# Kernel tuning notes

Measured on AMD Instinct MI355X. Metric: run time of the kernel, lower is better.

The kernel has to match this reference:

```python
import jax, jax.numpy as jnp
import numpy as np

B, ENC, T, DIM, VOCAB = 16, 512, 64, 768, 21128
SCALE = 1.0 / np.sqrt(DIM)
NEG = -1e30
EPS = 1e-6


def setup_inputs() -> dict:
    key = jax.random.key(0)
    ks = jax.random.split(key, 20)
    def lin(k, out_f, in_f):
        k1, k2 = jax.random.split(k)
        bound = 1.0 / np.sqrt(in_f)
        W = jax.random.uniform(k1, (out_f, in_f), jnp.float32, -bound, bound)
        b = jax.random.uniform(k2, (out_f,), jnp.float32, -bound, bound)
        return W, b
    W_r, b_r = lin(ks[5], DIM, 3 * DIM)
    W_u, b_u = lin(ks[6], DIM, 3 * DIM)
    W_c, b_c = lin(ks[7], DIM, 3 * DIM)
    W_out, b_out = lin(ks[8], DIM, DIM)
    W_copy, b_copy = lin(ks[9], DIM, DIM)
    W_mode, b_mode = lin(ks[10], 1, DIM)
    return {
        "input_ids": jax.random.randint(ks[0], (B, ENC), 0, VOCAB, dtype=jnp.int32),
        "input_context": jax.random.normal(ks[1], (B, ENC, DIM), jnp.float32),
        "context_mask": jnp.ones((B, ENC), jnp.float32),
        "decode_input": jax.random.randint(ks[2], (B, T), 0, VOCAB, dtype=jnp.int32),
        "decode_target": jax.random.randint(ks[3], (B, T), 0, VOCAB, dtype=jnp.int32),
        "use_beam_search": 0,
        "beam_width": 1,
        "emb_W": jax.random.normal(ks[4], (VOCAB, DIM), jnp.float32) * 0.02,
        "W_r": W_r, "b_r": b_r,
        "W_u": W_u, "b_u": b_u,
        "W_c": W_c, "b_c": b_c,
        "W_out": W_out, "b_out": b_out,
        "W_copy": W_copy, "b_copy": b_copy,
        "W_mode": W_mode, "b_mode": b_mode,
        "init_h": jax.random.normal(ks[11], (1, DIM), jnp.float32) * 0.02,
    }


def _decode(input_ids, input_context, context_mask, decode_emb, emb_W,
            W_r, b_r, W_u, b_u, W_c, b_c, W_out, b_out, W_copy, b_copy,
            W_mode, b_mode, init_h):
    mask_add = (1.0 - context_mask) * NEG  # (B, ENC)
    rows = jnp.arange(B)[:, None]

    def step(h, emb_t):
        # attention over encoder context
        score = jnp.einsum('bsd,bd->bs', input_context, h) * SCALE + mask_add
        attn = jax.nn.softmax(score, axis=-1)
        attn_vec = jnp.einsum('bs,bsd->bd', attn, input_context)
        x = jnp.concatenate([attn_vec, emb_t, h], axis=-1)  # (B, 3*DIM)
        r = jax.nn.sigmoid(x @ W_r.T + b_r)
        u = jax.nn.sigmoid(x @ W_u.T + b_u)
        xc = jnp.concatenate([attn_vec, emb_t, r * h], axis=-1)
        c = jnp.tanh(xc @ W_c.T + b_c)
        h_new = (1.0 - u) * h + u * c
        # generate distribution (tied embedding softmax)
        out = h_new @ W_out.T + b_out
        vocab_prob = jax.nn.softmax(out @ emb_W.T, axis=-1)  # (B, VOCAB)
        # copy distribution over source positions
        copy_q = h_new @ W_copy.T + b_copy
        copy_logits = jnp.einsum('bd,bsd->bs', copy_q, input_context) + mask_add
        input_prob = jax.nn.softmax(copy_logits, axis=-1)
        mode = jax.nn.sigmoid(h_new @ W_mode.T + b_mode)  # (B, 1)
        vp = vocab_prob * mode
        vp = vp.at[rows, input_ids].add(input_prob * (1.0 - mode))
        return h_new, vp

    h0 = jnp.broadcast_to(init_h, (B, DIM))
    _, probs = jax.lax.scan(step, h0, decode_emb)  # probs: (T, B, VOCAB)
    return probs


def reference(input_ids, input_context, context_mask, decode_input, decode_target,
              use_beam_search, beam_width, emb_W, W_r, b_r, W_u, b_u, W_c, b_c,
              W_out, b_out, W_copy, b_copy, W_mode, b_mode, init_h):
    decode_emb = jnp.transpose(emb_W[decode_input], (1, 0, 2))  # (T, B, DIM)
    probs = _decode(input_ids, input_context, context_mask, decode_emb, emb_W,
                    W_r, b_r, W_u, b_u, W_c, b_c, W_out, b_out, W_copy, b_copy,
                    W_mode, b_mode, init_h)
    predict = jnp.transpose(probs, (1, 0, 2)).reshape(-1, VOCAB)  # (B*T, VOCAB)
    tgt = decode_target.reshape(-1)
    p = predict[jnp.arange(tgt.shape[0]), tgt]
    nz = (tgt != 0).astype(jnp.float32)
    loss = jnp.sum(-jnp.log(p + EPS) * nz) / jnp.sum(nz)
    return jnp.full((B,), loss)
```

## Files before the change

### kernel.cpp

```cpp
#include <hip/hip_runtime.h>
#include <hip/hip_bf16.h>
#include <math.h>

#define Bdim 16
#define ENC 512
#define Tn 64
#define DIM 768
#define VOCAB 21128
#define SCALEF 0.03608439182435161f
#define NEGF   -1e30f
#define NBLK 256
#define DYN_LDS (100 * 1024)

__device__ __forceinline__ float wred_sum(float v) {
#pragma unroll
  for (int m = 32; m >= 1; m >>= 1) v += __shfl_xor(v, m, 64);
  return v;
}
__device__ __forceinline__ float sigmf(float x) { return 1.0f / (1.0f + __expf(-x)); }

__device__ __forceinline__ void astore(float* p, float v) {
  __hip_atomic_store(p, v, __ATOMIC_RELAXED, __HIP_MEMORY_SCOPE_AGENT);
}
__device__ __forceinline__ void astore2(float* p, float a, float b) {
  float2 v = make_float2(a, b);
  __hip_atomic_store((unsigned long long*)p, *(unsigned long long*)&v,
                     __ATOMIC_RELAXED, __HIP_MEMORY_SCOPE_AGENT);
}
__device__ __forceinline__ float aloadf(const float* p) {
  return __hip_atomic_load(const_cast<float*>(p), __ATOMIC_RELAXED, __HIP_MEMORY_SCOPE_AGENT);
}
__device__ __forceinline__ unsigned afadd(unsigned* p) {
  return __hip_atomic_fetch_add(p, 1u, __ATOMIC_RELAXED, __HIP_MEMORY_SCOPE_AGENT);
}
__device__ __forceinline__ unsigned aloadu(const unsigned* p) {
  return __hip_atomic_load(const_cast<unsigned*>(p), __ATOMIC_RELAXED, __HIP_MEMORY_SCOPE_AGENT);
}

__device__ __forceinline__ void gbar(unsigned* leaf, unsigned* root, int idx, int xcd) {
  __syncthreads();
  if (threadIdx.x == 0) {
    asm volatile("s_waitcnt vmcnt(0)" ::: "memory");
    unsigned prev = afadd(&leaf[(idx * 8 + xcd) * 16]);
    if (((prev + 1u) & 31u) == 0u) afadd(&root[idx * 16]);
    while (aloadu(&root[idx * 16]) < 8u) __builtin_amdgcn_s_sleep(1);
  }
  __syncthreads();
}
__device__ __forceinline__ void lbar(unsigned* lbc, int xcd, unsigned tgt) {
  __syncthreads();
  if (threadIdx.x == 0) {
    asm volatile("s_waitcnt vmcnt(0)" ::: "memory");
    afadd(&lbc[xcd * 16]);
    while (aloadu(&lbc[xcd * 16]) < tgt) __builtin_amdgcn_s_sleep(1);
  }
  __syncthreads();
}

__device__ __forceinline__ unsigned int f2bf(float f) {
  unsigned int u = __float_as_uint(f);
  u += 0x7fffu + ((u >> 16) & 1u);
  return u >> 16;
}
__device__ __forceinline__ float bflo(unsigned int p) { return __uint_as_float(p << 16); }
__device__ __forceinline__ float bfhi(unsigned int p) { return __uint_as_float(p & 0xffff0000u); }

__global__ void k_zero_coh(unsigned long long* __restrict__ p, int n64) {
  int i = blockIdx.x * blockDim.x + threadIdx.x;
  int st = gridDim.x * blockDim.x;
  for (; i < n64; i += st)
    __hip_atomic_store(&p[i], 0ULL, __ATOMIC_RELAXED, __HIP_MEMORY_SCOPE_AGENT);
}

__global__ void k_h0(const float* __restrict__ init_h, float* __restrict__ h_all) {
  int i = blockIdx.x * blockDim.x + threadIdx.x;
  if (i < Bdim * DIM) h_all[i] = init_h[i % DIM];
}

__global__ void __launch_bounds__(256, 2) k_pre(
    const int* __restrict__ din, const float* __restrict__ emb,
    const float* __restrict__ Wr, const float* __restrict__ br,
    const float* __restrict__ Wu, const float* __restrict__ bu,
    const float* __restrict__ Wc, const float* __restrict__ bc,
    float* __restrict__ P_ru, float* __restrict__ P_c) {
  const int nb = blockIdx.x, tbc = blockIdx.y;
  const int n = nb * 256 + threadIdx.x;
  const float* wrow;
  float bias;
  if (n < 768)       { wrow = Wr + n * 2304 + 768;          bias = br[n]; }
  else if (n < 1536) { wrow = Wu + (n - 768) * 2304 + 768;  bias = bu[n - 768]; }
  else               { wrow = Wc + (n - 1536) * 2304 + 768; bias = bc[n - 1536]; }
  int id[16];
#pragma unroll
  for (int i = 0; i < 16; ++i) {
    int row = tbc * 16 + i;
    id[i] = din[(row & 15) * Tn + (row >> 4)];
  }
  float acc[16];
#pragma unroll
  for (int i = 0; i < 16; ++i) acc[i] = bias;
  for (int k = 0; k < DIM; k += 4) {
    float4 w = *(const float4*)(wrow + k);
#pragma unroll
    for (int i = 0; i < 16; ++i) {
      float4 x = *(const float4*)(emb + (size_t)id[i] * DIM + k);
      acc[i] = fmaf(w.x, x.x, fmaf(w.y, x.y, fmaf(w.z, x.z, fmaf(w.w, x.w, acc[i]))));
    }
  }
#pragma unroll
  for (int i = 0; i < 16; ++i) {
    int row = tbc * 16 + i;
    if (n < 1536) P_ru[(size_t)row * 1536 + n] = acc[i];
    else          P_c[(size_t)row * 768 + (n - 1536)] = acc[i];
  }
}

__global__ void __launch_bounds__(512, 1) k_seq(
    const float* __restrict__ ctx, const float* __restrict__ mask,
    const float* __restrict__ Wr, const float* __restrict__ Wu,
    const float* __restrict__ Wc,
    const float* __restrict__ P_ru, const float* __restrict__ P_c,
    float* __restrict__ h_all, float* __restrict__ attnc,
    float* __restrict__ r_coh, float* __restrict__ pbuf,
    float* __restrict__ psum,
    unsigned* __restrict__ slotctr, unsigned* __restrict__ leaf,
    unsigned* __restrict__ root, unsigned* __restrict__ lbc) {
  extern __shared__ float dynpad[];
  float* ctx_lds = dynpad;
  float* e_lds   = dynpad + 24576;
  float* pred    = dynpad + 24576 + 32;
  float* psh     = dynpad + 24576 + 32 + 816;
  __shared__ int slot_sh;
  const int tid = threadIdx.x;
  const int lane = tid & 63;
  const int wv = tid >> 6;
  int xcd;
  asm volatile("s_getreg_b32 %0, hwreg(HW_REG_XCC_ID)" : "=s"(xcd));
  xcd &= 7;
  if (tid == 0) slot_sh = (int)afadd(&slotctr[xcd * 16]);
  __syncthreads();
  const int slot = slot_sh;
  const int gid = xcd * 32 + slot;
  const int bA = 2 * xcd + (slot & 1);
  const int chunk = slot >> 1;
  const int dsl = chunk * 48;
  const int rg0 = gid * 3;
  const int cg0 = gid * 3;
  const int b0 = 2 * wv;

  {
    const float* chunkbase = ctx + ((size_t)(bA * ENC + chunk * 32)) * DIM;
#pragma unroll
    for (int k = 0; k < 12; ++k) {
      const int f = k * 2048 + tid * 4;
      *(float4*)(ctx_lds + f) = *(const float4*)(chunkbase + f);
    }
  }

  unsigned int wreg[9][12];
#pragma unroll
  for (int i = 0; i < 9; ++i) {
    const float* src = (i < 3) ? (Wr + (size_t)(rg0 + i) * 2304)
                     : (i < 6) ? (Wu + (size_t)(cg0 + i - 3) * 2304)
                               : (Wc + (size_t)(cg0 + i - 6) * 2304);
#pragma unroll
    for (int j = 0; j < 6; ++j) {
      int xcol = 4 * lane + 256 * j;
      int scol = (j < 3) ? xcol : (1536 + xcol - 768);
      float4 v = *(const float4*)(src + scol);
      wreg[i][2 * j]     = (f2bf(v.x)) | (f2bf(v.y) << 16);
      wreg[i][2 * j + 1] = (f2bf(v.z)) | (f2bf(v.w) << 16);
    }
  }
  float madd[4];
#pragma unroll
  for (int i = 0; i < 4; ++i)
    madd[i] = (1.0f - mask[bA * ENC + chunk * 32 + 4 * wv + i]) * NEGF;

  __syncthreads();

  int bidx = 0;
  for (int t = 0; t < Tn; ++t) {
    {
      const float* hrow = h_all + (size_t)(t * Bdim + bA) * DIM;
      float hreg[12];
#pragma unroll
      for (int j = 0; j < 12; ++j) hreg[j] = hrow[lane + 64 * j];
#pragma unroll
      for (int i = 0; i < 4; ++i) {
        const int rr = 4 * wv + i;
        const float* crow = ctx_lds + rr * 768;
        float dot = 0.f;
#pragma unroll
        for (int j = 0; j < 12; ++j) dot = fmaf(crow[lane + 64 * j], hreg[j], dot);
        dot = wred_sum(dot);
        if (lane == 0) e_lds[rr] = __expf(fmaf(dot, SCALEF, madd[i]));
      }
    }
    __syncthreads();

    if (wv == 0) {
      float ev = (lane < 32) ? e_lds[lane] : 0.f;
      float es = wred_sum(ev);
      if (lane == 0) astore(&psum[bA * 16 + chunk], es);
    }
    if (tid < 384) {
      const int d0 = 2 * tid;
      float a0 = 0.f, a1 = 0.f;
#pragma unroll 8
      for (int r = 0; r < 32; ++r) {
        const float e = e_lds[r];
        const float2 c2 = *(const float2*)(ctx_lds + r * 768 + d0);
        a0 = fmaf(e, c2.x, a0);
        a1 = fmaf(e, c2.y, a1);
      }
      astore2(&pbuf[(size_t)(bA * 16 + chunk) * 768 + d0], a0, a1);
    }
    lbar(lbc, xcd, 32u * (unsigned)(t + 1));

    {
      const int p1 = tid >> 5, o1 = tid & 31;
      float v1 = aloadf(&pbuf[(size_t)(bA * 16 + p1) * 768 + dsl + o1]);
      float v2 = 0.f;
      int p2 = 0, o2 = 0;
      if (tid < 256) {
        p2 = tid >> 4; o2 = 32 + (tid & 15);
        v2 = aloadf(&pbuf[(size_t)(bA * 16 + p2) * 768 + dsl + o2]);
      }
      if (tid < 16) psh[tid] = aloadf(&psum[bA * 16 + tid]);
      pred[o1 * 17 + p1] = v1;
      if (tid < 256) pred[o2 * 17 + p2] = v2;
      __syncthreads();
      if (tid < 48) {
        float s = 0.f, den = 0.f;
#pragma unroll
        for (int p = 0; p < 16; ++p) { s += pred[tid * 17 + p]; den += psh[p]; }
        astore(&attnc[(size_t)(t * Bdim + bA) * DIM + dsl + tid], s / den);
      }
    }
    gbar(leaf, root, bidx++, xcd);

    float4 xv[2][6];
#pragma unroll
    for (int bb = 0; bb < 2; ++bb) {
      const int b = b0 + bb;
      const float* ab = attnc + (size_t)(t * Bdim + b) * DIM;
      const float* hb = h_all + (size_t)(t * Bdim + b) * DIM;
#pragma unroll
      for (int j = 0; j < 3; ++j)
        xv[bb][j] = *(const float4*)(ab + 4 * lane + 256 * j);
#pragma unroll
      for (int j = 0; j < 3; ++j)
        xv[bb][3 + j] = *(const float4*)(hb + 4 * lane + 256 * j);
    }
    float u_reg[3];
#pragma unroll
    for (int i = 0; i < 3; ++i) {
      float d0 = 0.f, d1 = 0.f;
#pragma unroll
      for (int j = 0; j < 6; ++j) {
        const unsigned int p0 = wreg[i][2 * j], p1 = wreg[i][2 * j + 1];
        const float w0 = bflo(p0), w1 = bfhi(p0), w2 = bflo(p1), w3 = bfhi(p1);
        d0 = fmaf(w0, xv[0][j].x, fmaf(w1, xv[0][j].y, fmaf(w2, xv[0][j].z, fmaf(w3, xv[0][j].w, d0))));
        d1 = fmaf(w0, xv[1][j].x, fmaf(w1, xv[1][j].y, fmaf(w2, xv[1][j].z, fmaf(w3, xv[1][j].w, d1))));
      }
      d0 = wred_sum(d0);
      d1 = wred_sum(d1);
      if (lane < 2) {
        const int b = b0 + lane;
        const int row = rg0 + i;
        const float s = sigmf(P_ru[(size_t)(t * Bdim + b) * 1536 + row] + (lane ? d1 : d0));
        astore(&r_coh[(size_t)(t * Bdim + b) * DIM + row], s);
      }
    }
#pragma unroll
    for (int i = 0; i < 3; ++i) {
      float d0 = 0.f, d1 = 0.f;
#pragma unroll
      for (int j = 0; j < 6; ++j) {
        const unsigned int p0 = wreg[3 + i][2 * j], p1 = wreg[3 + i][2 * j + 1];
        const float w0 = bflo(p0), w1 = bfhi(p0), w2 = bflo(p1), w3 = bfhi(p1);
        d0 = fmaf(w0, xv[0][j].x, fmaf(w1, xv[0][j].y, fmaf(w2, xv[0][j].z, fmaf(w3, xv[0][j].w, d0))));
        d1 = fmaf(w0, xv[1][j].x, fmaf(w1, xv[1][j].y, fmaf(w2, xv[1][j].z, fmaf(w3, xv[1][j].w, d1))));
      }
      d0 = wred_sum(d0);
      d1 = wred_sum(d1);
      if (lane < 2) {
        const int b = b0 + lane;
        u_reg[i] = sigmf(P_ru[(size_t)(t * Bdim + b) * 1536 + 768 + cg0 + i] + (lane ? d1 : d0));
      }
    }
    gbar(leaf, root, bidx++, xcd);

#pragma unroll
    for (int bb = 0; bb < 2; ++bb) {
      const int b = b0 + bb;
      const float* rb = r_coh + (size_t)(t * Bdim + b) * DIM;
#pragma unroll
      for (int j = 0; j < 3; ++j) {
        float4 rv = *(const float4*)(rb + 4 * lane + 256 * j);
        xv[bb][3 + j].x *= rv.x; xv[bb][3 + j].y *= rv.y;
        xv[bb][3 + j].z *= rv.z; xv[bb][3 + j].w *= rv.w;
      }
    }
#pragma unroll
    for (int i = 0; i < 3; ++i) {
      float d0 = 0.f, d1 = 0.f;
#pragma unroll
      for (int j = 0; j < 6; ++j) {
        const unsigned int p0 = wreg[6 + i][2 * j], p1 = wreg[6 + i][2 * j + 1];
        const float w0 = bflo(p0), w1 = bfhi(p0), w2 = bflo(p1), w3 = bfhi(p1);
        d0 = fmaf(w0, xv[0][j].x, fmaf(w1, xv[0][j].y, fmaf(w2, xv[0][j].z, fmaf(w3, xv[0][j].w, d0))));
        d1 = fmaf(w0, xv[1][j].x, fmaf(w1, xv[1][j].y, fmaf(w2, xv[1][j].z, fmaf(w3, xv[1][j].w, d1))));
      }
      d0 = wred_sum(d0);
      d1 = wred_sum(d1);
      if (lane < 2) {
        const int b = b0 + lane;
        const int row = cg0 + i;
        const float c = tanhf(P_c[(size_t)(t * Bdim + b) * DIM + row] + (lane ? d1 : d0));
        const float hp = h_all[(size_t)(t * Bdim + b) * DIM + row];
        astore(&h_all[(size_t)((t + 1) * Bdim + b) * DIM + row], hp + u_reg[i] * (c - hp));
      }
    }
    gbar(leaf, root, bidx++, xcd);
  }
}

__global__ void __launch_bounds__(256, 2) k_out(
    const float* __restrict__ Wo, const float* __restrict__ bo,
    const float* __restrict__ Wcp, const float* __restrict__ bcp,
    const float* __restrict__ h_all, float* __restrict__ out_all,
    float* __restrict__ copyq) {
  const int nb = blockIdx.x, tbc = blockIdx.y;
  const int n = nb * 256 + threadIdx.x;
  const float* wrow;
  float bias;
  if (n < 768) { wrow = Wo + (size_t)n * 768;          bias = bo[n]; }
  else         { wrow = Wcp + (size_t)(n - 768) * 768; bias = bcp[n - 768]; }
  const float* hbase = h_all + (size_t)(tbc * 16 + 16) * DIM;
  float acc[16];
#pragma unroll
  for (int i = 0; i < 16; ++i) acc[i] = bias;
  for (int k = 0; k < DIM; k += 4) {
    float4 w = *(const float4*)(wrow + k);
#pragma unroll
    for (int i = 0; i < 16; ++i) {
      float4 x = *(const float4*)(hbase + i * DIM + k);
      acc[i] = fmaf(w.x, x.x, fmaf(w.y, x.y, fmaf(w.z, x.z, fmaf(w.w, x.w, acc[i]))));
    }
  }
#pragma unroll
  for (int i = 0; i < 16; ++i) {
    int row = tbc * 16 + i;
    if (n < 768) out_all[(size_t)row * 768 + n] = acc[i];
    else         copyq[(size_t)row * 768 + (n - 768)] = acc[i];
  }
}

__global__ void __launch_bounds__(512, 2) k_copy(
    const int* __restrict__ ids, const int* __restrict__ dtg,
    const float* __restrict__ ctx, const float* __restrict__ mask,
    const float* __restrict__ copyq,
    float* __restrict__ cnum, float* __restrict__ cden) {
  const int sc = blockIdx.x, b = blockIdx.y;
  const int lane = threadIdx.x & 63;
  const int seg = __builtin_amdgcn_readfirstlane(threadIdx.x >> 6);
  const int s = sc * 64 + lane;
  __shared__ float part[8][64];
  float creg[96];
  const float* crow = ctx + ((size_t)(b * ENC + s)) * DIM + seg * 96;
#pragma unroll
  for (int kk = 0; kk < 96; kk += 4) {
    float4 v = *(const float4*)(crow + kk);
    creg[kk] = v.x; creg[kk + 1] = v.y; creg[kk + 2] = v.z; creg[kk + 3] = v.w;
  }
  const float madd = (1.0f - mask[b * ENC + s]) * NEGF;
  const int myid = ids[b * ENC + s];
  for (int t = 0; t < Tn; ++t) {
    const int row = t * Bdim + b;
    const float* q = copyq + (size_t)row * 768 + seg * 96;
    float dot = 0.f;
#pragma unroll
    for (int kk = 0; kk < 96; kk += 4) {
      float4 qv = *(const float4*)(q + kk);
      dot = fmaf(qv.x, creg[kk], fmaf(qv.y, creg[kk + 1],
            fmaf(qv.z, creg[kk + 2], fmaf(qv.w, creg[kk + 3], dot))));
    }
    part[seg][lane] = dot;
    __syncthreads();
    if (threadIdx.x < 64) {
      float logit = madd;
#pragma unroll
      for (int w = 0; w < 8; ++w) logit += part[w][lane];
      float e = __expf(logit);
      int tgt = dtg[b * Tn + t];
      float ne = (myid == tgt) ? e : 0.f;
      float dsum = wred_sum(e);
      float nsum = wred_sum(ne);
      if (lane == 0) {
        atomicAdd(&cden[row], dsum);
        if (nsum != 0.f) atomicAdd(&cnum[row], nsum);
      }
    }
    __syncthreads();
  }
}

__global__ void __launch_bounds__(256, 1) k_vocab(
    const float* __restrict__ emb, const float* __restrict__ out_all,
    float* __restrict__ S) {
  const int vc = blockIdx.x, tbc = blockIdx.y;
  const int tb0 = tbc * 32;
  const int v = vc * 256 + threadIdx.x;
  const bool valid = v < VOCAB;
  const int vv = valid ? v : 0;
  float acc[32];
#pragma unroll
  for (int i = 0; i < 32; ++i) acc[i] = 0.f;
  const float* erow = emb + (size_t)vv * DIM;
  for (int k = 0; k < DIM; k += 4) {
    float4 w = *(const float4*)(erow + k);
#pragma unroll
    for (int i = 0; i < 32; ++i) {
      float4 a = *(const float4*)(out_all + (size_t)(tb0 + i) * DIM + k);
      acc[i] = fmaf(w.x, a.x, fmaf(w.y, a.y, fmaf(w.z, a.z, fmaf(w.w, a.w, acc[i]))));
    }
  }
  __shared__ float rowsum[32];
  if (threadIdx.x < 32) rowsum[threadIdx.x] = 0.f;
  __syncthreads();
  const int lane = threadIdx.x & 63;
#pragma unroll
  for (int i = 0; i < 32; ++i) {
    float e = valid ? __expf(acc[i]) : 0.f;
    float r = wred_sum(e);
    if (lane == 0) atomicAdd(&rowsum[i], r);
  }
  __syncthreads();
  if (threadIdx.x < 32) atomicAdd(&S[tb0 + threadIdx.x], rowsum[threadIdx.x]);
}

__global__ void k_tgt(
    const int* __restrict__ dtg, const float* __restrict__ out_all,
    const float* __restrict__ emb, const float* __restrict__ Wm,
    const float* __restrict__ bm, const float* __restrict__ h_all,
    const float* __restrict__ S, const float* __restrict__ cnum,
    const float* __restrict__ cden, float* __restrict__ loss) {
  const int lane = threadIdx.x & 63;
  const int w = __builtin_amdgcn_readfirstlane(threadIdx.x >> 6);
  for (int rr = 0; rr < 16; ++rr) {
    const int row = (blockIdx.x * 4 + w) * 16 + rr;
    const int t = row >> 4, b = row & 15;
    const int tgt = dtg[b * Tn + t];
    const float* orow = out_all + (size_t)row * DIM + lane * 12;
    const float* erow = emb + (size_t)tgt * DIM + lane * 12;
    const float* hrow = h_all + (size_t)(row + 16) * DIM + lane * 12;
    const float* wm = Wm + lane * 12;
    float lt = 0.f, md = 0.f;
#pragma unroll
    for (int k = 0; k < 12; k += 4) {
      float4 o = *(const float4*)(orow + k);
      float4 e = *(const float4*)(erow + k);
      float4 h = *(const float4*)(hrow + k);
      float4 m = *(const float4*)(wm + k);
      lt = fmaf(o.x, e.x, fmaf(o.y, e.y, fmaf(o.z, e.z, fmaf(o.w, e.w, lt))));
      md = fmaf(m.x, h.x, fmaf(m.y, h.y, fmaf(m.z, h.z, fmaf(m.w, h.w, md))));
    }
    lt = wred_sum(lt);
    md = wred_sum(md);
    if (lane == 0 && tgt != 0) {
      float mode = sigmf(md + bm[0]);
      float pv = __expf(lt) / S[row] * mode;
      float den = cden[row];
      float pc = (den > 0.f) ? (cnum[row] / den) : 0.f;
      float p = pv + (1.0f - mode) * pc;
      atomicAdd(&loss[0], -logf(p + 1e-6f));
      atomicAdd(&loss[1], 1.0f);
    }
  }
}

__global__ void k_write(const float* __restrict__ loss, float* __restrict__ out) {
  if (threadIdx.x < Bdim) out[threadIdx.x] = loss[0] / loss[1];
}

extern "C" void kernel_launch(void* const* d_in, const int* in_sizes, int n_in,
                              void* d_out, int out_size, void* d_ws, size_t ws_size,
                              hipStream_t stream) {
  (void)in_sizes; (void)n_in; (void)out_size; (void)ws_size;
  const int*   input_ids = (const int*)d_in[0];
  const float* ctx       = (const float*)d_in[1];
  const float* cmask     = (const float*)d_in[2];
  const int*   din       = (const int*)d_in[3];
  const int*   dtg       = (const int*)d_in[4];
  const float* embW      = (const float*)d_in[7];
  const float* Wr = (const float*)d_in[8];  const float* br  = (const float*)d_in[9];
  const float* Wu = (const float*)d_in[10]; const float* bu  = (const float*)d_in[11];
  const float* Wc = (const float*)d_in[12]; const float* bc  = (const float*)d_in[13];
  const float* Wo = (const float*)d_in[14]; const float* bo  = (const float*)d_in[15];
  const float* Wcp= (const float*)d_in[16]; const float* bcp = (const float*)d_in[17];
  const float* Wm = (const float*)d_in[18]; const float* bm  = (const float*)d_in[19];
  const float* ih = (const float*)d_in[20];

  float* ws      = (float*)d_ws;
  float* P_ru    = ws;
  float* P_c     = P_ru + 1024 * 1536;
  float* h_all   = P_c + 1024 * 768;
  float* out_all = h_all + 65 * 16 * 768;
  float* copyq   = out_all + 1024 * 768;
  float* attnc   = copyq + 1024 * 768;
  float* r_coh   = attnc + 64 * 16 * 768;
  float* pbuf    = r_coh + 64 * 16 * 768;
  float* psum    = pbuf + 16 * 16 * 768;
  float* S       = psum + 256;
  float* cnum    = S + 1024;
  float* cden    = cnum + 1024;
  float* loss    = cden + 1024;
  unsigned* slotctr = (unsigned*)(loss + 32);
  unsigned* leaf    = slotctr + 8 * 16;
  unsigned* root    = leaf + 192 * 8 * 16;
  unsigned* lbc     = root + 192 * 16;
  const int nzero64 = (3 * 1024 + 32 + 8 * 16 + 192 * 8 * 16 + 192 * 16 + 8 * 16) / 2;

  hipFuncSetAttribute((const void*)k_seq,
                      hipFuncAttributeMaxDynamicSharedMemorySize, DYN_LDS);

  k_zero_coh<<<64, 1024, 0, stream>>>((unsigned long long*)S, nzero64);
  k_h0<<<12, 1024, 0, stream>>>(ih, h_all);
  k_pre<<<dim3(9, 64), 256, 0, stream>>>(din, embW, Wr, br, Wu, bu, Wc, bc, P_ru, P_c);

  k_seq<<<NBLK, 512, DYN_LDS, stream>>>(ctx, cmask, Wr, Wu, Wc, P_ru, P_c,
                                        h_all, attnc, r_coh, pbuf, psum,
                                        slotctr, leaf, root, lbc);

  k_out<<<dim3(6, 64), 256, 0, stream>>>(Wo, bo, Wcp, bcp, h_all, out_all, copyq);
  k_copy<<<dim3(8, 16), 512, 0, stream>>>(input_ids, dtg, ctx, cmask, copyq, cnum, cden);
  k_vocab<<<dim3(83, 32), 256, 0, stream>>>(embW, out_all, S);
  k_tgt<<<16, 256, 0, stream>>>(dtg, out_all, embW, Wm, bm, h_all, S, cnum, cden, loss);
  k_write<<<1, 64, 0, stream>>>(loss, (float*)d_out);
}
```

Before: 4.286 ms.

## Tighten persistent GRU step barriers, hoist loads, and overlap candidate-gate work

The barrier poll now runs on two waves with no sleep and signals through an LDS flag. Intra-XCD partial sums are written with workgroup-scope stores and read back with sc0 loads that target L2. Per-step loads of h, the P_ru/P_c biases and the previous h are hoisted ahead of the attention phase. The attention half of the candidate-gate dot product is computed before the r barrier, so only the r*h half remains after it. Lane indices are rotated per block to spread accesses across banks and channels. The gains come from shorter critical-path latency, at the risk of heavier spin traffic and weaker memory-scope guarantees.

```diff
diff --git a/kernel.cpp b/kernel.cpp
--- a/kernel.cpp
+++ b/kernel.cpp
@@ -22,39 +22,66 @@
 __device__ __forceinline__ void astore(float* p, float v) {
   __hip_atomic_store(p, v, __ATOMIC_RELAXED, __HIP_MEMORY_SCOPE_AGENT);
 }
-__device__ __forceinline__ void astore2(float* p, float a, float b) {
+__device__ __forceinline__ unsigned afadd(unsigned* p) {
+  return __hip_atomic_fetch_add(p, 1u, __ATOMIC_RELAXED, __HIP_MEMORY_SCOPE_AGENT);
+}
+__device__ __forceinline__ unsigned aloadu(const unsigned* p) {
+  return __hip_atomic_load(const_cast<unsigned*>(p), __ATOMIC_RELAXED, __HIP_MEMORY_SCOPE_AGENT);
+}
+
+__device__ __forceinline__ void wstore(float* p, float v) {
+  __hip_atomic_store(p, v, __ATOMIC_RELAXED, __HIP_MEMORY_SCOPE_WORKGROUP);
+}
+__device__ __forceinline__ void wstore2(float* p, float a, float b) {
   float2 v = make_float2(a, b);
   __hip_atomic_store((unsigned long long*)p, *(unsigned long long*)&v,
-                     __ATOMIC_RELAXED, __HIP_MEMORY_SCOPE_AGENT);
-}
-__device__ __forceinline__ float aloadf(const float* p) {
-  return __hip_atomic_load(const_cast<float*>(p), __ATOMIC_RELAXED, __HIP_MEMORY_SCOPE_AGENT);
-}
-__device__ __forceinline__ unsigned afadd(unsigned* p) {
-  return __hip_atomic_fetch_add(p, 1u, __ATOMIC_RELAXED, __HIP_MEMORY_SCOPE_AGENT);
-}
-__device__ __forceinline__ unsigned aloadu(const unsigned* p) {
-  return __hip_atomic_load(const_cast<unsigned*>(p), __ATOMIC_RELAXED, __HIP_MEMORY_SCOPE_AGENT);
-}
-
-__device__ __forceinline__ void gbar(unsigned* leaf, unsigned* root, int idx, int xcd) {
+                     __ATOMIC_RELAXED, __HIP_MEMORY_SCOPE_WORKGROUP);
+}
+__device__ __forceinline__ float l2ldf(const float* p) {
+  unsigned u;
+  asm volatile("global_load_dword %0, %1, off sc0\n\ts_waitcnt vmcnt(0)"
+               : "=&v"(u) : "v"(p) : "memory");
+  return __uint_as_float(u);
+}
+__device__ __forceinline__ float2 l2ldf2(const float* p) {
+  unsigned long long u;
+  asm volatile("global_load_dwordx2 %0, %1, off sc0\n\ts_waitcnt vmcnt(0)"
+               : "=&v"(u) : "v"(p) : "memory");
+  return make_float2(__uint_as_float((unsigned)u),
+                     __uint_as_float((unsigned)(u >> 32)));
+}
+
+__device__ __forceinline__ void mpoll(const unsigned* p, unsigned tgt,
+                                      volatile int* done) {
+  const int lane = threadIdx.x & 63;
+  const int wv = threadIdx.x >> 6;
+  if (lane == 0 && wv < 2) {
+    while (*done == 0) {
+      if (aloadu(p) >= tgt) *done = 1;
+    }
+  }
+  __syncthreads();
+}
+__device__ __forceinline__ void gbar(unsigned* leaf, unsigned* root, int idx,
+                                     int xcd, volatile int* done) {
+  if (threadIdx.x == 0) *done = 0;
   __syncthreads();
   if (threadIdx.x == 0) {
     asm volatile("s_waitcnt vmcnt(0)" ::: "memory");
     unsigned prev = afadd(&leaf[(idx * 8 + xcd) * 16]);
     if (((prev + 1u) & 31u) == 0u) afadd(&root[idx * 16]);
-    while (aloadu(&root[idx * 16]) < 8u) __builtin_amdgcn_s_sleep(1);
-  }
-  __syncthreads();
-}
-__device__ __forceinline__ void lbar(unsigned* lbc, int xcd, unsigned tgt) {
+  }
+  mpoll(&root[idx * 16], 8u, done);
+}
+__device__ __forceinline__ void lbar(unsigned* lbc, int xcd, unsigned tgt,
+                                     volatile int* done) {
+  if (threadIdx.x == 0) *done = 0;
   __syncthreads();
   if (threadIdx.x == 0) {
     asm volatile("s_waitcnt vmcnt(0)" ::: "memory");
     afadd(&lbc[xcd * 16]);
-    while (aloadu(&lbc[xcd * 16]) < tgt) __builtin_amdgcn_s_sleep(1);
-  }
-  __syncthreads();
+  }
+  mpoll(&lbc[xcd * 16], tgt, done);
 }
 
 __device__ __forceinline__ unsigned int f2bf(float f) {
@@ -131,6 +158,7 @@
   float* pred    = dynpad + 24576 + 32;
   float* psh     = dynpad + 24576 + 32 + 816;
   __shared__ int slot_sh;
+  __shared__ int done_sh;
   const int tid = threadIdx.x;
   const int lane = tid & 63;
   const int wv = tid >> 6;
@@ -147,6 +175,9 @@
   const int rg0 = gid * 3;
   const int cg0 = gid * 3;
   const int b0 = 2 * wv;
+  const int rl  = (lane + 2 * slot) & 63;
+  const int rl1 = (lane + 4 * chunk) & 63;
+  volatile int* done = &done_sh;
 
   {
     const float* chunkbase = ctx + ((size_t)(bA * ENC + chunk * 32)) * DIM;
@@ -165,7 +196,7 @@
                                : (Wc + (size_t)(cg0 + i - 6) * 2304);
 #pragma unroll
     for (int j = 0; j < 6; ++j) {
-      int xcol = 4 * lane + 256 * j;
+      int xcol = 4 * rl + 256 * j;
       int scol = (j < 3) ? xcol : (1536 + xcol - 768);
       float4 v = *(const float4*)(src + scol);
       wreg[i][2 * j]     = (f2bf(v.x)) | (f2bf(v.y) << 16);
@@ -181,18 +212,38 @@
 
   int bidx = 0;
   for (int t = 0; t < Tn; ++t) {
+    float4 xvh[2][3];
+#pragma unroll
+    for (int bb = 0; bb < 2; ++bb) {
+      const float* hb = h_all + (size_t)(t * Bdim + b0 + bb) * DIM;
+#pragma unroll
+      for (int j = 0; j < 3; ++j)
+        xvh[bb][j] = *(const float4*)(hb + 4 * rl + 256 * j);
+    }
+    float Pr3[3], Pu3[3], Pc3[3], hp3[3];
+    if (lane < 2) {
+      const int b = b0 + lane;
+#pragma unroll
+      for (int i = 0; i < 3; ++i) {
+        Pr3[i] = P_ru[(size_t)(t * Bdim + b) * 1536 + rg0 + i];
+        Pu3[i] = P_ru[(size_t)(t * Bdim + b) * 1536 + 768 + cg0 + i];
+        Pc3[i] = P_c[(size_t)(t * Bdim + b) * DIM + cg0 + i];
+        hp3[i] = h_all[(size_t)(t * Bdim + b) * DIM + cg0 + i];
+      }
+    }
+
     {
       const float* hrow = h_all + (size_t)(t * Bdim + bA) * DIM;
       float hreg[12];
 #pragma unroll
-      for (int j = 0; j < 12; ++j) hreg[j] = hrow[lane + 64 * j];
+      for (int j = 0; j < 12; ++j) hreg[j] = hrow[rl1 + 64 * j];
 #pragma unroll
       for (int i = 0; i < 4; ++i) {
         const int rr = 4 * wv + i;
         const float* crow = ctx_lds + rr * 768;
         float dot = 0.f;
 #pragma unroll
-        for (int j = 0; j < 12; ++j) dot = fmaf(crow[lane + 64 * j], hreg[j], dot);
+        for (int j = 0; j < 12; ++j) dot = fmaf(crow[rl1 + 64 * j], hreg[j], dot);
         dot = wred_sum(dot);
         if (lane == 0) e_lds[rr] = __expf(fmaf(dot, SCALEF, madd[i]));
       }
@@ -202,7 +253,7 @@
     if (wv == 0) {
       float ev = (lane < 32) ? e_lds[lane] : 0.f;
       float es = wred_sum(ev);
-      if (lane == 0) astore(&psum[bA * 16 + chunk], es);
+      if (lane == 0) wstore(&psum[bA * 16 + chunk], es);
     }
     if (tid < 384) {
       const int d0 = 2 * tid;
@@ -214,22 +265,19 @@
         a0 = fmaf(e, c2.x, a0);
         a1 = fmaf(e, c2.y, a1);
       }
-      astore2(&pbuf[(size_t)(bA * 16 + chunk) * 768 + d0], a0, a1);
-    }
-    lbar(lbc, xcd, 32u * (unsigned)(t + 1));
+      wstore2(&pbuf[(size_t)(bA * 16 + chunk) * 768 + d0], a0, a1);
+    }
+    lbar(lbc, xcd, 32u * (unsigned)(t + 1), done);
 
     {
-      const int p1 = tid >> 5, o1 = tid & 31;
-      float v1 = aloadf(&pbuf[(size_t)(bA * 16 + p1) * 768 + dsl + o1]);
-      float v2 = 0.f;
-      int p2 = 0, o2 = 0;
-      if (tid < 256) {
-        p2 = tid >> 4; o2 = 32 + (tid & 15);
-        v2 = aloadf(&pbuf[(size_t)(bA * 16 + p2) * 768 + dsl + o2]);
-      }
-      if (tid < 16) psh[tid] = aloadf(&psum[bA * 16 + tid]);
-      pred[o1 * 17 + p1] = v1;
-      if (tid < 256) pred[o2 * 17 + p2] = v2;
+      const int ch = tid >> 5, d2 = tid & 31;
+      if (d2 < 24) {
+        float2 v = l2ldf2(&pbuf[(size_t)(bA * 16 + ch) * 768 + dsl + 2 * d2]);
+        pred[(2 * d2) * 17 + ch] = v.x;
+        pred[(2 * d2 + 1) * 17 + ch] = v.y;
+      } else if (d2 == 24) {
+        psh[ch] = l2ldf(&psum[bA * 16 + ch]);
+      }
       __syncthreads();
       if (tid < 48) {
         float s = 0.f, den = 0.f;
@@ -238,22 +286,17 @@
         astore(&attnc[(size_t)(t * Bdim + bA) * DIM + dsl + tid], s / den);
       }
     }
-    gbar(leaf, root, bidx++, xcd);
-
-    float4 xv[2][6];
+    gbar(leaf, root, bidx++, xcd, done);
+
+    float4 xv[2][3];
 #pragma unroll
     for (int bb = 0; bb < 2; ++bb) {
-      const int b = b0 + bb;
-      const float* ab = attnc + (size_t)(t * Bdim + b) * DIM;
-      const float* hb = h_all + (size_t)(t * Bdim + b) * DIM;
+      const float* ab = attnc + (size_t)(t * Bdim + b0 + bb) * DIM;
 #pragma unroll
       for (int j = 0; j < 3; ++j)
-        xv[bb][j] = *(const float4*)(ab + 4 * lane + 256 * j);
-#pragma unroll
-      for (int j = 0; j < 3; ++j)
-        xv[bb][3 + j] = *(const float4*)(hb + 4 * lane + 256 * j);
-    }
-    float u_reg[3];
+        xv[bb][j] = *(const float4*)(ab + 4 * rl + 256 * j);
+    }
+    float u_reg[3], ca0[3], ca1[3];
 #pragma unroll
     for (int i = 0; i < 3; ++i) {
       float d0 = 0.f, d1 = 0.f;
@@ -261,69 +304,75 @@
       for (int j = 0; j < 6; ++j) {
         const unsigned int p0 = wreg[i][2 * j], p1 = wreg[i][2 * j + 1];
         const float w0 = bflo(p0), w1 = bfhi(p0), w2 = bflo(p1), w3 = bfhi(p1);
-        d0 = fmaf(w0, xv[0][j].x, fmaf(w1, xv[0][j].y, fmaf(w2, xv[0][j].z, fmaf(w3, xv[0][j].w, d0))));
-        d1 = fmaf(w0, xv[1][j].x, fmaf(w1, xv[1][j].y, fmaf(w2, xv[1][j].z, fmaf(w3, xv[1][j].w, d1))));
+        const float4 x0 = (j < 3) ? xv[0][j] : xvh[0][j - 3];
+        const float4 x1 = (j < 3) ? xv[1][j] : xvh[1][j - 3];
+        d0 = fmaf(w0, x0.x, fmaf(w1, x0.y, fmaf(w2, x0.z, fmaf(w3, x0.w, d0))));
+        d1 = fmaf(w0, x1.x, fmaf(w1, x1.y, fmaf(w2, x1.z, fmaf(w3, x1.w, d1))));
       }
       d0 = wred_sum(d0);
       d1 = wred_sum(d1);
       if (lane < 2) {
-        const int b = b0 + lane;
-        const int row = rg0 + i;
-        const float s = sigmf(P_ru[(size_t)(t * Bdim + b) * 1536 + row] + (lane ? d1 : d0));
-        astore(&r_coh[(size_t)(t * Bdim + b) * DIM + row], s);
+        const float s = sigmf(Pr3[i] + (lane ? d1 : d0));
+        astore(&r_coh[(size_t)(t * Bdim + b0 + lane) * DIM + rg0 + i], s);
       }
     }
 #pragma unroll
     for (int i = 0; i < 3; ++i) {
-      float d0 = 0.f, d1 = 0.f;
+      float d0 = 0.f, d1 = 0.f, c0 = 0.f, c1 = 0.f;
 #pragma unroll
       for (int j = 0; j < 6; ++j) {
         const unsigned int p0 = wreg[3 + i][2 * j], p1 = wreg[3 + i][2 * j + 1];
         const float w0 = bflo(p0), w1 = bfhi(p0), w2 = bflo(p1), w3 = bfhi(p1);
-        d0 = fmaf(w0, xv[0][j].x, fmaf(w1, xv[0][j].y, fmaf(w2, xv[0][j].z, fmaf(w3, xv[0][j].w, d0))));
-        d1 = fmaf(w0, xv[1][j].x, fmaf(w1, xv[1][j].y, fmaf(w2, xv[1][j].z, fmaf(w3, xv[1][j].w, d1))));
+        const float4 x0 = (j < 3) ? xv[0][j] : xvh[0][j - 3];
+        const float4 x1 = (j < 3) ? xv[1][j] : xvh[1][j - 3];
+        d0 = fmaf(w0, x0.x, fmaf(w1, x0.y, fmaf(w2, x0.z, fmaf(w3, x0.w, d0))));
+        d1 = fmaf(w0, x1.x, fmaf(w1, x1.y, fmaf(w2, x1.z, fmaf(w3, x1.w, d1))));
+      }
+#pragma unroll
+      for (int j = 0; j < 3; ++j) {
+        const unsigned int p0 = wreg[6 + i][2 * j], p1 = wreg[6 + i][2 * j + 1];
+        const float w0 = bflo(p0), w1 = bfhi(p0), w2 = bflo(p1), w3 = bfhi(p1);
+        c0 = fmaf(w0, xv[0][j].x, fmaf(w1, xv[0][j].y, fmaf(w2, xv[0][j].z, fmaf(w3, xv[0][j].w, c0))));
+        c1 = fmaf(w0, xv[1][j].x, fmaf(w1, xv[1][j].y, fmaf(w2, xv[1][j].z, fmaf(w3, xv[1][j].w, c1))));
+      }
+      d0 = wred_sum(d0);
+      d1 = wred_sum(d1);
+      if (lane < 2) u_reg[i] = sigmf(Pu3[i] + (lane ? d1 : d0));
+      ca0[i] = c0;
+      ca1[i] = c1;
+    }
+    gbar(leaf, root, bidx++, xcd, done);
+
+    float4 vh[2][3];
+#pragma unroll
+    for (int bb = 0; bb < 2; ++bb) {
+      const float* rb = r_coh + (size_t)(t * Bdim + b0 + bb) * DIM;
+#pragma unroll
+      for (int j = 0; j < 3; ++j) {
+        float4 rv = *(const float4*)(rb + 4 * rl + 256 * j);
+        vh[bb][j] = make_float4(xvh[bb][j].x * rv.x, xvh[bb][j].y * rv.y,
+                                xvh[bb][j].z * rv.z, xvh[bb][j].w * rv.w);
+      }
+    }
+#pragma unroll
+    for (int i = 0; i < 3; ++i) {
+      float d0 = ca0[i], d1 = ca1[i];
+#pragma unroll
+      for (int j = 0; j < 3; ++j) {
+        const unsigned int p0 = wreg[6 + i][2 * (3 + j)], p1 = wreg[6 + i][2 * (3 + j) + 1];
+        const float w0 = bflo(p0), w1 = bfhi(p0), w2 = bflo(p1), w3 = bfhi(p1);
+        d0 = fmaf(w0, vh[0][j].x, fmaf(w1, vh[0][j].y, fmaf(w2, vh[0][j].z, fmaf(w3, vh[0][j].w, d0))));
+        d1 = fmaf(w0, vh[1][j].x, fmaf(w1, vh[1][j].y, fmaf(w2, vh[1][j].z, fmaf(w3, vh[1][j].w, d1))));
       }
       d0 = wred_sum(d0);
       d1 = wred_sum(d1);
       if (lane < 2) {
-        const int b = b0 + lane;
-        u_reg[i] = sigmf(P_ru[(size_t)(t * Bdim + b) * 1536 + 768 + cg0 + i] + (lane ? d1 : d0));
-      }
-    }
-    gbar(leaf, root, bidx++, xcd);
-
-#pragma unroll
-    for (int bb = 0; bb < 2; ++bb) {
-      const int b = b0 + bb;
-      const float* rb = r_coh + (size_t)(t * Bdim + b) * DIM;
-#pragma unroll
-      for (int j = 0; j < 3; ++j) {
-        float4 rv = *(const float4*)(rb + 4 * lane + 256 * j);
-        xv[bb][3 + j].x *= rv.x; xv[bb][3 + j].y *= rv.y;
-        xv[bb][3 + j].z *= rv.z; xv[bb][3 + j].w *= rv.w;
-      }
-    }
-#pragma unroll
-    for (int i = 0; i < 3; ++i) {
-      float d0 = 0.f, d1 = 0.f;
-#pragma unroll
-      for (int j = 0; j < 6; ++j) {
-        const unsigned int p0 = wreg[6 + i][2 * j], p1 = wreg[6 + i][2 * j + 1];
-        const float w0 = bflo(p0), w1 = bfhi(p0), w2 = bflo(p1), w3 = bfhi(p1);
-        d0 = fmaf(w0, xv[0][j].x, fmaf(w1, xv[0][j].y, fmaf(w2, xv[0][j].z, fmaf(w3, xv[0][j].w, d0))));
-        d1 = fmaf(w0, xv[1][j].x, fmaf(w1, xv[1][j].y, fmaf(w2, xv[1][j].z, fmaf(w3, xv[1][j].w, d1))));
-      }
-      d0 = wred_sum(d0);
-      d1 = wred_sum(d1);
-      if (lane < 2) {
-        const int b = b0 + lane;
-        const int row = cg0 + i;
-        const float c = tanhf(P_c[(size_t)(t * Bdim + b) * DIM + row] + (lane ? d1 : d0));
-        const float hp = h_all[(size_t)(t * Bdim + b) * DIM + row];
-        astore(&h_all[(size_t)((t + 1) * Bdim + b) * DIM + row], hp + u_reg[i] * (c - hp));
-      }
-    }
-    gbar(leaf, root, bidx++, xcd);
+        const float c = tanhf(Pc3[i] + (lane ? d1 : d0));
+        astore(&h_all[(size_t)((t + 1) * Bdim + b0 + lane) * DIM + cg0 + i],
+               hp3[i] + u_reg[i] * (c - hp3[i]));
+      }
+    }
+    gbar(leaf, root, bidx++, xcd, done);
   }
 }
 
```

Result: faster. 4.141 ms (-3.4%).
